# Performance work log

Hardware: AMD Instinct MI355X
Metric: run time of the kernel (lower is better)

## Reference

```python
import jax, jax.numpy as jnp
import numpy as np

N_NODES = 100000

def setup_inputs() -> dict:
    key = jax.random.key(0)
    ks = jax.random.split(key, 9)
    d_in, d_out, e_dim, E = 64, 64, 16, 1600000
    x = jax.random.normal(ks[0], (N_NODES, d_in), dtype=jnp.float32)
    edge_index = jax.random.randint(ks[1], (2, E), 0, N_NODES, dtype=jnp.int64)
    edge_attr = jax.random.normal(ks[2], (E, e_dim), dtype=jnp.float32)
    s = 0.1
    W_edge = jax.random.normal(ks[3], (e_dim, d_in), dtype=jnp.float32) * s
    b_edge = jax.random.normal(ks[4], (d_in,), dtype=jnp.float32) * s
    W1 = jax.random.normal(ks[5], (d_in, d_out), dtype=jnp.float32) * s
    b1 = jax.random.normal(ks[6], (d_out,), dtype=jnp.float32) * s
    W2 = jax.random.normal(ks[7], (d_out, d_out), dtype=jnp.float32) * s
    b2 = jax.random.normal(ks[8], (d_out,), dtype=jnp.float32) * s
    return {"x": x, "edge_index": edge_index, "edge_attr": edge_attr,
            "W_edge": W_edge, "b_edge": b_edge, "W1": W1, "b1": b1,
            "W2": W2, "b2": b2}

def reference(x, edge_index, edge_attr, W_edge, b_edge, W1, b1, W2, b2):
    eps = 0.0
    src, dst = edge_index[0], edge_index[1]
    # project edge features to node dim (GINEConv lin with edge_dim set)
    e = edge_attr @ W_edge + b_edge                 # [E, d_in]
    msg = jax.nn.relu(x[src] + e)                   # gather + add + ReLU
    aggr = jax.ops.segment_sum(msg, dst, num_segments=N_NODES)  # scatter-sum
    h = (1.0 + eps) * x + aggr                      # [N, d_in]
    # 2-layer MLP update
    return jax.nn.relu(h @ W1 + b1) @ W2 + b2
```

## Files before the change

kernel.cpp:

```cpp
#include <hip/hip_runtime.h>
#include <hip/hip_fp16.h>

#define D 64
#define EDIM 16
#define CAP 64

#define T_A    2048
#define BSHIFT 9
#define BRANGE 512
#define BCAP   9216

__global__ __launch_bounds__(256) void convert_x_kernel(
    const float* __restrict__ x, __half* __restrict__ xh, int n4)
{
    int i = blockIdx.x * blockDim.x + threadIdx.x;
    const int stride = gridDim.x * blockDim.x;
    for (; i < n4; i += stride) {
        const float4 v = ((const float4*)x)[i];
        __half2 a = __float22half2_rn(make_float2(v.x, v.y));
        __half2 b = __float22half2_rn(make_float2(v.z, v.w));
        uint2 u;
        u.x = *(unsigned*)&a;
        u.y = *(unsigned*)&b;
        ((uint2*)xh)[i] = u;
    }
}

__global__ __launch_bounds__(256) void coarse_bin_kernel(
    const int* __restrict__ dst, const int* __restrict__ src,
    long long* __restrict__ coarse, int* __restrict__ gcursor, int E)
{
    __shared__ long long      stage[T_A];
    __shared__ unsigned short stage_b[T_A];
    __shared__ int lcnt[256];
    __shared__ int loff[256];
    __shared__ int lbase[256];
    __shared__ int s_valid;

    const int t    = threadIdx.x;
    const int base = blockIdx.x * T_A;

    lcnt[t] = 0;
    __syncthreads();

    int       myb[8];
    int       myslot[8];
    long long myrec[8];
#pragma unroll
    for (int j = 0; j < 8; ++j) {
        const int i = base + t + j * 256;
        if (i < E) {
            const int d = dst[i];
            const int s = src[i];
            const int b = d >> BSHIFT;
            myb[j]   = b;
            myrec[j] = (long long)(unsigned)s
                     | ((long long)i << 17)
                     | ((long long)(d & (BRANGE - 1)) << 38);
            myslot[j] = atomicAdd(&lcnt[b], 1);
        } else {
            myb[j] = -1;
        }
    }
    __syncthreads();

    const int v = lcnt[t];
    loff[t] = v;
    __syncthreads();
    for (int off = 1; off < 256; off <<= 1) {
        const int add = (t >= off) ? loff[t - off] : 0;
        __syncthreads();
        loff[t] += add;
        __syncthreads();
    }
    if (t == 255) s_valid = loff[255];
    const int excl = loff[t] - v;
    loff[t] = excl;
    if (v > 0) lbase[t] = atomicAdd(&gcursor[t * 16], v);
    else       lbase[t] = 0;
    __syncthreads();

#pragma unroll
    for (int j = 0; j < 8; ++j) {
        if (myb[j] >= 0) {
            const int p = loff[myb[j]] + myslot[j];
            stage[p]   = myrec[j];
            stage_b[p] = (unsigned short)myb[j];
        }
    }
    __syncthreads();

    const int nv = s_valid;
    for (int p = t; p < nv; p += 256) {
        const int b   = stage_b[p];
        const int rel = lbase[b] + (p - loff[b]);
        if (rel < BCAP)
            coarse[(size_t)b * BCAP + rel] = stage[p];
    }
}

__global__ __launch_bounds__(1024) void refine_csr_kernel(
    const long long* __restrict__ coarse, const int* __restrict__ gcursor,
    int2* __restrict__ rec, int2* __restrict__ meta, int N, int kc)
{
    extern __shared__ long long dense[];
    __shared__ int lc[BRANGE];
    __shared__ int bs[BRANGE];
    __shared__ int gb[256];

    const int t = threadIdx.x;
    const int b = blockIdx.x;

    if (t < BRANGE) lc[t] = 0;
    if (t < 256) gb[t] = (t < kc) ? min(gcursor[t * 16], BCAP) : 0;
    __syncthreads();

    for (int off = 1; off < 256; off <<= 1) {
        int add = 0;
        if (t < 256 && t >= off) add = gb[t - off];
        __syncthreads();
        if (t < 256) gb[t] += add;
        __syncthreads();
    }
    const int bstart = (b == 0) ? 0 : gb[b - 1];
    const int m      = min(gcursor[b * 16], BCAP);
    const long long* crs = coarse + (size_t)b * BCAP;

    long long rp[9];
    int       rslot[9];
    int       rdlo[9];
    int       nmine = 0;
#pragma unroll
    for (int j = 0; j < 9; ++j) {
        const int i = t + j * 1024;
        if (i < m) {
            const long long p = crs[i];
            const int dlo = (int)((p >> 38) & (BRANGE - 1));
            rp[j]    = p;
            rdlo[j]  = dlo;
            rslot[j] = atomicAdd(&lc[dlo], 1);
            nmine    = j + 1;
        }
    }
    __syncthreads();

    if (t < BRANGE) bs[t] = lc[t];
    __syncthreads();
    for (int off = 1; off < BRANGE; off <<= 1) {
        int add = 0;
        if (t < BRANGE && t >= off) add = bs[t - off];
        __syncthreads();
        if (t < BRANGE) bs[t] += add;
        __syncthreads();
    }
    if (t < BRANGE) bs[t] -= lc[t];
    __syncthreads();

#pragma unroll
    for (int j = 0; j < 9; ++j) {
        if (j < nmine)
            dense[bs[rdlo[j]] + rslot[j]] = rp[j];
    }
    __syncthreads();

    for (int i = t; i < m; i += 1024) {
        const long long p = dense[i];
        rec[bstart + i] =
            make_int2((int)(p & 0x1FFFF), (int)((p >> 17) & 0x1FFFFF));
    }
    if (t < BRANGE) {
        const int node = (b << BSHIFT) + t;
        if (node < N) meta[node] = make_int2(bstart + bs[t], lc[t]);
    }
}

__global__ __launch_bounds__(256, 4) void gather_mlp_kernel(
    const float*  __restrict__ x,
    const __half* __restrict__ xh,
    const int2*   __restrict__ rec,
    const int2*   __restrict__ meta,
    const float*  __restrict__ edge_attr,
    const float*  __restrict__ W_edge,
    const float*  __restrict__ b_edge,
    const float* __restrict__ W1, const float* __restrict__ b1,
    const float* __restrict__ W2, const float* __restrict__ b2,
    float*       __restrict__ out,
    int N)
{
    __shared__ float W1s[D * D];
    __shared__ float W2s[D * D];
    __shared__ float hstage[4][D];
    __shared__ float tstage[4][D];

    const int t = threadIdx.x;
    {
        const float4* w1v = (const float4*)W1;
        const float4* w2v = (const float4*)W2;
        float4* w1s = (float4*)W1s;
        float4* w2s = (float4*)W2s;
#pragma unroll
        for (int i = 0; i < 4; ++i) {
            w1s[t + i * 256] = w1v[t + i * 256];
            w2s[t + i * 256] = w2v[t + i * 256];
        }
    }
    __syncthreads();

    const int lane = t & 63;
    const int u    = lane >> 4;
    const int c    = lane & 15;
    const int wv   = t >> 6;
    const int wave   = blockIdx.x * 4 + wv;
    const int nwaves = gridDim.x * 4;

    float4 we[EDIM];
#pragma unroll
    for (int k = 0; k < EDIM; ++k)
        we[k] = *(const float4*)(W_edge + k * D + 4 * c);
    const float4 be  = *(const float4*)(b_edge + 4 * c);
    const float  b1v = b1[lane];
    const float  b2v = b2[lane];

    for (int n = wave; n < N; n += nwaves) {
        const int2 md  = meta[n];
        const int  deg = md.y;
        const int2* bucket = rec + md.x;
        float4 acc = make_float4(0.0f, 0.0f, 0.0f, 0.0f);

        for (int e = 0; e < deg; e += 4) {
            const int   ee  = e + u;
            const bool  ok  = ee < deg;
            const int   ec  = ok ? ee : (deg - 1);
            const float msk = ok ? 1.0f : 0.0f;

            const int2 r = bucket[ec];

            const uint2 xu = *(const uint2*)(xh + (size_t)r.x * D + 4 * c);
            const float2 f01 = __half22float2(*(const __half2*)&xu.x);
            const float2 f23 = __half22float2(*(const __half2*)&xu.y);

            const float4* ap = (const float4*)(edge_attr + (size_t)r.y * EDIM);
            const float4 a0 = ap[0], a1 = ap[1], a2 = ap[2], a3 = ap[3];
            const float av[EDIM] = {a0.x, a0.y, a0.z, a0.w,
                                    a1.x, a1.y, a1.z, a1.w,
                                    a2.x, a2.y, a2.z, a2.w,
                                    a3.x, a3.y, a3.z, a3.w};
            float4 v = be;
#pragma unroll
            for (int k = 0; k < EDIM; ++k) {
                v.x = fmaf(av[k], we[k].x, v.x);
                v.y = fmaf(av[k], we[k].y, v.y);
                v.z = fmaf(av[k], we[k].z, v.z);
                v.w = fmaf(av[k], we[k].w, v.w);
            }
            acc.x = fmaf(fmaxf(f01.x + v.x, 0.0f), msk, acc.x);
            acc.y = fmaf(fmaxf(f01.y + v.y, 0.0f), msk, acc.y);
            acc.z = fmaf(fmaxf(f23.x + v.z, 0.0f), msk, acc.z);
            acc.w = fmaf(fmaxf(f23.y + v.w, 0.0f), msk, acc.w);
        }

#pragma unroll
        for (int off = 16; off < 64; off <<= 1) {
            acc.x += __shfl_xor(acc.x, off, 64);
            acc.y += __shfl_xor(acc.y, off, 64);
            acc.z += __shfl_xor(acc.z, off, 64);
            acc.w += __shfl_xor(acc.w, off, 64);
        }

        if (u == 0) {
            const float4 xn = *(const float4*)(x + (size_t)n * D + 4 * c);
            float4 o;
            o.x = xn.x + acc.x;
            o.y = xn.y + acc.y;
            o.z = xn.z + acc.z;
            o.w = xn.w + acc.w;
            *(float4*)(&hstage[wv][4 * c]) = o;
        }
        asm volatile("s_waitcnt lgkmcnt(0)" ::: "memory");

        float acc1 = b1v;
#pragma unroll
        for (int k = 0; k < D; k += 4) {
            const float4 hv = *(const float4*)(&hstage[wv][k]);
            acc1 = fmaf(hv.x, W1s[(k + 0) * D + lane], acc1);
            acc1 = fmaf(hv.y, W1s[(k + 1) * D + lane], acc1);
            acc1 = fmaf(hv.z, W1s[(k + 2) * D + lane], acc1);
            acc1 = fmaf(hv.w, W1s[(k + 3) * D + lane], acc1);
        }
        tstage[wv][lane] = fmaxf(acc1, 0.0f);
        asm volatile("s_waitcnt lgkmcnt(0)" ::: "memory");

        float acc2 = b2v;
#pragma unroll
        for (int k = 0; k < D; k += 4) {
            const float4 tv = *(const float4*)(&tstage[wv][k]);
            acc2 = fmaf(tv.x, W2s[(k + 0) * D + lane], acc2);
            acc2 = fmaf(tv.y, W2s[(k + 1) * D + lane], acc2);
            acc2 = fmaf(tv.z, W2s[(k + 2) * D + lane], acc2);
            acc2 = fmaf(tv.w, W2s[(k + 3) * D + lane], acc2);
        }
        out[(size_t)n * D + lane] = acc2;
        asm volatile("s_waitcnt lgkmcnt(0)" ::: "memory");
    }
}

__global__ __launch_bounds__(256) void mlp_kernel(
    const float* __restrict__ W1, const float* __restrict__ b1,
    const float* __restrict__ W2, const float* __restrict__ b2,
    float* inout, int N)
{
    __shared__ float W1s[D * D];
    __shared__ float W2s[D * D];
    __shared__ float hbuf[4][D];
    __shared__ float tbuf[4][D];

    const int t = threadIdx.x;
    const float4* w1v = (const float4*)W1;
    const float4* w2v = (const float4*)W2;
    float4* w1s = (float4*)W1s;
    float4* w2s = (float4*)W2s;
#pragma unroll
    for (int i = 0; i < 4; ++i) {
        w1s[t + i * 256] = w1v[t + i * 256];
        w2s[t + i * 256] = w2v[t + i * 256];
    }
    __syncthreads();

    const int lane = t & 63;
    const int wv   = t >> 6;
    const float b1v = b1[lane];
    const float b2v = b2[lane];

    for (int base = blockIdx.x * 4; base < N; base += gridDim.x * 4) {
        const int    node = base + wv;
        const size_t off  = (size_t)node * D + lane;

        hbuf[wv][lane] = inout[off];
        __syncthreads();

        float acc = b1v;
#pragma unroll
        for (int k = 0; k < D; k += 4) {
            const float4 hv = *(const float4*)(&hbuf[wv][k]);
            acc = fmaf(hv.x, W1s[(k + 0) * D + lane], acc);
            acc = fmaf(hv.y, W1s[(k + 1) * D + lane], acc);
            acc = fmaf(hv.z, W1s[(k + 2) * D + lane], acc);
            acc = fmaf(hv.w, W1s[(k + 3) * D + lane], acc);
        }
        tbuf[wv][lane] = fmaxf(acc, 0.0f);
        __syncthreads();

        float acc2 = b2v;
#pragma unroll
        for (int k = 0; k < D; k += 4) {
            const float4 tv = *(const float4*)(&tbuf[wv][k]);
            acc2 = fmaf(tv.x, W2s[(k + 0) * D + lane], acc2);
            acc2 = fmaf(tv.y, W2s[(k + 1) * D + lane], acc2);
            acc2 = fmaf(tv.z, W2s[(k + 2) * D + lane], acc2);
            acc2 = fmaf(tv.w, W2s[(k + 3) * D + lane], acc2);
        }
        inout[off] = acc2;
        __syncthreads();
    }
}

__global__ __launch_bounds__(256) void edge_atomic_kernel(
    const float* __restrict__ x,
    const int*   __restrict__ src,
    const int*   __restrict__ dst,
    const float* __restrict__ edge_attr,
    const float* __restrict__ W_edge,
    const float* __restrict__ b_edge,
    float*       __restrict__ aggr,
    int E)
{
    const int lane   = threadIdx.x & 63;
    const int wave   = blockIdx.x * 4 + (threadIdx.x >> 6);
    const int nwaves = gridDim.x * 4;

    float we[EDIM];
#pragma unroll
    for (int k = 0; k < EDIM; ++k) we[k] = W_edge[k * D + lane];
    const float be = b_edge[lane];

    for (int i = wave; i < E; i += nwaves) {
        const int s = src[i];
        const int d = dst[i];
        const float4* eap = (const float4*)(edge_attr + (size_t)i * EDIM);
        float acc = be;
#pragma unroll
        for (int c = 0; c < 4; ++c) {
            const float4 ea = eap[c];
            acc = fmaf(ea.x, we[4 * c + 0], acc);
            acc = fmaf(ea.y, we[4 * c + 1], acc);
            acc = fmaf(ea.z, we[4 * c + 2], acc);
            acc = fmaf(ea.w, we[4 * c + 3], acc);
        }
        float m = fmaxf(x[(size_t)s * D + lane] + acc, 0.0f);
        atomicAdd(&aggr[(size_t)d * D + lane], m);
    }
}

__global__ __launch_bounds__(256) void add_x_kernel(
    const float* __restrict__ x, float* __restrict__ h, size_t n)
{
    size_t i = (size_t)blockIdx.x * blockDim.x + threadIdx.x;
    size_t stride = (size_t)gridDim.x * blockDim.x;
    for (; i < n; i += stride) h[i] += x[i];
}

extern "C" void kernel_launch(void* const* d_in, const int* in_sizes, int n_in,
                              void* d_out, int out_size, void* d_ws, size_t ws_size,
                              hipStream_t stream)
{
    const float* x      = (const float*)d_in[0];
    const int*   eidx   = (const int*)d_in[1];
    const float* eattr  = (const float*)d_in[2];
    const float* W_edge = (const float*)d_in[3];
    const float* b_edge = (const float*)d_in[4];
    const float* W1     = (const float*)d_in[5];
    const float* b1     = (const float*)d_in[6];
    const float* W2     = (const float*)d_in[7];
    const float* b2     = (const float*)d_in[8];
    float*       out    = (float*)d_out;

    const int E = in_sizes[1] / 2;
    const int N = in_sizes[0] / D;

    const int* src = eidx;
    const int* dst = eidx + E;

    const int kc = (N + BRANGE - 1) >> BSHIFT;

    const size_t sz_rec    = (size_t)E * sizeof(int2);
    const size_t sz_coarse = (size_t)kc * BCAP * sizeof(long long);
    const size_t sz_xh     = (size_t)N * D * sizeof(__half);
    const size_t sz_meta   = (size_t)N * sizeof(int2);
    const size_t sz_gcur   = 256 * 16 * sizeof(int);
    const size_t need      = sz_rec + sz_coarse + sz_xh + sz_meta + sz_gcur;

    if (ws_size >= need) {
        char* p = (char*)d_ws;
        int2*      rec     = (int2*)p;                      p += sz_rec;
        long long* coarse  = (long long*)p;                 p += sz_coarse;
        __half*    xh      = (__half*)p;                    p += sz_xh;
        int2*      meta    = (int2*)p;                      p += sz_meta;
        int*       gcursor = (int*)p;

        hipMemsetAsync(gcursor, 0, sz_gcur, stream);
        convert_x_kernel<<<1024, 256, 0, stream>>>(x, xh, N * D / 4);
        const int gridA = (E + T_A - 1) / T_A;
        coarse_bin_kernel<<<gridA, 256, 0, stream>>>(dst, src, coarse, gcursor, E);
        refine_csr_kernel<<<kc, 1024, BCAP * sizeof(long long), stream>>>(
            coarse, gcursor, rec, meta, N, kc);
        gather_mlp_kernel<<<4096, 256, 0, stream>>>(x, xh, rec, meta,
                                                    eattr, W_edge, b_edge,
                                                    W1, b1, W2, b2, out, N);
    } else {
        hipMemsetAsync(out, 0, (size_t)N * D * sizeof(float), stream);
        edge_atomic_kernel<<<2048, 256, 0, stream>>>(x, src, dst, eattr,
                                                     W_edge, b_edge, out, E);
        add_x_kernel<<<1024, 256, 0, stream>>>(x, out, (size_t)N * D);
        mlp_kernel<<<2048, 256, 0, stream>>>(W1, b1, W2, b2, out, N);
    }
}
```

Baseline: 410.2 us.

## Permute edge_attr into CSR order as fp16 during refine, drop rec indirection

```diff
diff --git a/kernel.cpp b/kernel.cpp
--- a/kernel.cpp
+++ b/kernel.cpp
@@ -101,7 +101,9 @@
 
 __global__ __launch_bounds__(1024) void refine_csr_kernel(
     const long long* __restrict__ coarse, const int* __restrict__ gcursor,
-    int2* __restrict__ rec, int2* __restrict__ meta, int N, int kc)
+    const float* __restrict__ edge_attr,
+    int* __restrict__ srcs, __half* __restrict__ ea16,
+    int2* __restrict__ meta, int N, int kc)
 {
     extern __shared__ long long dense[];
     __shared__ int lc[BRANGE];
@@ -165,8 +167,28 @@
 
     for (int i = t; i < m; i += 1024) {
         const long long p = dense[i];
-        rec[bstart + i] =
-            make_int2((int)(p & 0x1FFFF), (int)((p >> 17) & 0x1FFFFF));
+        const int s   = (int)(p & 0x1FFFF);
+        const int eid = (int)((p >> 17) & 0x1FFFFF);
+        srcs[bstart + i] = s;
+
+        const float4* ap = (const float4*)(edge_attr + (size_t)eid * EDIM);
+        const float4 a0 = ap[0], a1 = ap[1], a2 = ap[2], a3 = ap[3];
+        __half2 h0 = __float22half2_rn(make_float2(a0.x, a0.y));
+        __half2 h1 = __float22half2_rn(make_float2(a0.z, a0.w));
+        __half2 h2 = __float22half2_rn(make_float2(a1.x, a1.y));
+        __half2 h3 = __float22half2_rn(make_float2(a1.z, a1.w));
+        __half2 h4 = __float22half2_rn(make_float2(a2.x, a2.y));
+        __half2 h5 = __float22half2_rn(make_float2(a2.z, a2.w));
+        __half2 h6 = __float22half2_rn(make_float2(a3.x, a3.y));
+        __half2 h7 = __float22half2_rn(make_float2(a3.z, a3.w));
+        uint4 q0, q1;
+        q0.x = *(unsigned*)&h0; q0.y = *(unsigned*)&h1;
+        q0.z = *(unsigned*)&h2; q0.w = *(unsigned*)&h3;
+        q1.x = *(unsigned*)&h4; q1.y = *(unsigned*)&h5;
+        q1.z = *(unsigned*)&h6; q1.w = *(unsigned*)&h7;
+        uint4* dst16 = (uint4*)(ea16 + (size_t)(bstart + i) * EDIM);
+        dst16[0] = q0;
+        dst16[1] = q1;
     }
     if (t < BRANGE) {
         const int node = (b << BSHIFT) + t;
@@ -177,9 +199,9 @@
 __global__ __launch_bounds__(256, 4) void gather_mlp_kernel(
     const float*  __restrict__ x,
     const __half* __restrict__ xh,
-    const int2*   __restrict__ rec,
+    const int*    __restrict__ srcs,
+    const __half* __restrict__ ea16,
     const int2*   __restrict__ meta,
-    const float*  __restrict__ edge_attr,
     const float*  __restrict__ W_edge,
     const float*  __restrict__ b_edge,
     const float* __restrict__ W1, const float* __restrict__ b1,
@@ -224,7 +246,6 @@
     for (int n = wave; n < N; n += nwaves) {
         const int2 md  = meta[n];
         const int  deg = md.y;
-        const int2* bucket = rec + md.x;
         float4 acc = make_float4(0.0f, 0.0f, 0.0f, 0.0f);
 
         for (int e = 0; e < deg; e += 4) {
@@ -232,19 +253,28 @@
             const bool  ok  = ee < deg;
             const int   ec  = ok ? ee : (deg - 1);
             const float msk = ok ? 1.0f : 0.0f;
-
-            const int2 r = bucket[ec];
-
-            const uint2 xu = *(const uint2*)(xh + (size_t)r.x * D + 4 * c);
+            const int   pos = md.x + ec;
+
+            const int s = srcs[pos];
+
+            const uint2 xu = *(const uint2*)(xh + (size_t)s * D + 4 * c);
             const float2 f01 = __half22float2(*(const __half2*)&xu.x);
             const float2 f23 = __half22float2(*(const __half2*)&xu.y);
 
-            const float4* ap = (const float4*)(edge_attr + (size_t)r.y * EDIM);
-            const float4 a0 = ap[0], a1 = ap[1], a2 = ap[2], a3 = ap[3];
-            const float av[EDIM] = {a0.x, a0.y, a0.z, a0.w,
-                                    a1.x, a1.y, a1.z, a1.w,
-                                    a2.x, a2.y, a2.z, a2.w,
-                                    a3.x, a3.y, a3.z, a3.w};
+            const uint4* eap = (const uint4*)(ea16 + (size_t)pos * EDIM);
+            const uint4 q0 = eap[0], q1 = eap[1];
+            const float2 e0 = __half22float2(*(const __half2*)&q0.x);
+            const float2 e1 = __half22float2(*(const __half2*)&q0.y);
+            const float2 e2 = __half22float2(*(const __half2*)&q0.z);
+            const float2 e3 = __half22float2(*(const __half2*)&q0.w);
+            const float2 e4 = __half22float2(*(const __half2*)&q1.x);
+            const float2 e5 = __half22float2(*(const __half2*)&q1.y);
+            const float2 e6 = __half22float2(*(const __half2*)&q1.z);
+            const float2 e7 = __half22float2(*(const __half2*)&q1.w);
+            const float av[EDIM] = {e0.x, e0.y, e1.x, e1.y,
+                                    e2.x, e2.y, e3.x, e3.y,
+                                    e4.x, e4.y, e5.x, e5.y,
+                                    e6.x, e6.y, e7.x, e7.y};
             float4 v = be;
 #pragma unroll
             for (int k = 0; k < EDIM; ++k) {
@@ -432,18 +462,20 @@
 
     const int kc = (N + BRANGE - 1) >> BSHIFT;
 
-    const size_t sz_rec    = (size_t)E * sizeof(int2);
+    const size_t sz_ea16   = (size_t)E * EDIM * sizeof(__half);
     const size_t sz_coarse = (size_t)kc * BCAP * sizeof(long long);
     const size_t sz_xh     = (size_t)N * D * sizeof(__half);
+    const size_t sz_srcs   = (size_t)E * sizeof(int);
     const size_t sz_meta   = (size_t)N * sizeof(int2);
     const size_t sz_gcur   = 256 * 16 * sizeof(int);
-    const size_t need      = sz_rec + sz_coarse + sz_xh + sz_meta + sz_gcur;
+    const size_t need = sz_ea16 + sz_coarse + sz_xh + sz_srcs + sz_meta + sz_gcur;
 
     if (ws_size >= need) {
         char* p = (char*)d_ws;
-        int2*      rec     = (int2*)p;                      p += sz_rec;
+        __half*    ea16    = (__half*)p;                    p += sz_ea16;
         long long* coarse  = (long long*)p;                 p += sz_coarse;
         __half*    xh      = (__half*)p;                    p += sz_xh;
+        int*       srcs    = (int*)p;                       p += sz_srcs;
         int2*      meta    = (int2*)p;                      p += sz_meta;
         int*       gcursor = (int*)p;
 
@@ -452,9 +484,9 @@
         const int gridA = (E + T_A - 1) / T_A;
         coarse_bin_kernel<<<gridA, 256, 0, stream>>>(dst, src, coarse, gcursor, E);
         refine_csr_kernel<<<kc, 1024, BCAP * sizeof(long long), stream>>>(
-            coarse, gcursor, rec, meta, N, kc);
-        gather_mlp_kernel<<<4096, 256, 0, stream>>>(x, xh, rec, meta,
-                                                    eattr, W_edge, b_edge,
+            coarse, gcursor, eattr, srcs, ea16, meta, N, kc);
+        gather_mlp_kernel<<<4096, 256, 0, stream>>>(x, xh, srcs, ea16, meta,
+                                                    W_edge, b_edge,
                                                     W1, b1, W2, b2, out, N);
     } else {
         hipMemsetAsync(out, 0, (size_t)N * D * sizeof(float), stream);
```

New measurement: 400.6 us. 2.3% less time.
